# Kernel optimization log

Measured on AMD Instinct MI355X. Metric: run time of the kernel, lower is better.

## Reference

```python
import jax, jax.numpy as jnp
import numpy as np


def lga_once(x, w, r):
    """One pass of local guided aggregation (GANet LGA).

    x: [B, D, H, W] cost volume
    w: [B, 3*k*k, H, W] per-pixel guidance weights (k = 2r+1); the three
       k*k groups weight disparity planes d, d-1, d+1 respectively.
    out[b,d,h,w] = sum_{i,j in kxk window}
        w0[b,ij,h,w] * x[b, d,   h+i-r, w+j-r]
      + w1[b,ij,h,w] * x[b, d-1, h+i-r, w+j-r]
      + w2[b,ij,h,w] * x[b, d+1, h+i-r, w+j-r]
    with zero padding outside spatial and disparity bounds.
    """
    B, D, H, W = x.shape
    k = 2 * r + 1
    k2 = k * k
    w0 = w[:, 0 * k2:1 * k2]
    w1 = w[:, 1 * k2:2 * k2]
    w2 = w[:, 2 * k2:3 * k2]
    # disparity-shifted volumes: xm[:, d] = x[:, d-1], xp[:, d] = x[:, d+1]
    xm = jnp.pad(x, ((0, 0), (1, 0), (0, 0), (0, 0)))[:, :D]
    xp = jnp.pad(x, ((0, 0), (0, 1), (0, 0), (0, 0)))[:, 1:]
    spad = ((0, 0), (0, 0), (r, r), (r, r))
    x0p = jnp.pad(x, spad)
    xmp = jnp.pad(xm, spad)
    xpp = jnp.pad(xp, spad)
    out = jnp.zeros_like(x)
    idx = 0
    for i in range(k):          # small fixed kxk loop; data dims stay vectorized
        for j in range(k):
            p0 = x0p[:, :, i:i + H, j:j + W]
            pm = xmp[:, :, i:i + H, j:j + W]
            pp = xpp[:, :, i:i + H, j:j + W]
            out = out + (w0[:, idx:idx + 1] * p0
                         + w1[:, idx:idx + 1] * pm
                         + w2[:, idx:idx + 1] * pp)
            idx += 1
    return out


def setup_inputs() -> dict:
    key = jax.random.key(0)
    k1, k2 = jax.random.split(key)
    B, D, H, W = 2, 48, 320, 640
    r = 2
    kk = 2 * r + 1
    input1 = jax.random.normal(k1, (B, D, H, W), dtype=jnp.float32)
    input2 = jax.random.uniform(k2, (B, 3 * kk * kk, H, W), dtype=jnp.float32)
    return {"input1": input1, "input2": input2, "radius": r}


def reference(input1, input2, radius):
    # LGA2 = local guided aggregation applied twice with the same weights
    y = lga_once(input1, input2, radius)
    return lga_once(y, input2, radius)
```

## Files before the change

### kernel.cpp

```cpp
#include <hip/hip_runtime.h>

namespace {
constexpr int Bn = 2, Dn = 48, Hn = 320, Wn = 640;
constexpr int R = 2, K = 5, K2 = 25, C3 = 75;
constexpr int TW = 64, TH = 4;
constexpr int LW = TW + 2 * R;
constexpr int LH = TH + 2 * R;
constexpr int NT = TW * TH;
constexpr int LTOT = LH * LW;
constexpr int NCH = 3;
constexpr int NSLOT = 4;
}

__global__ __launch_bounds__(NT, 2)
void lga_pass(const float* __restrict__ x, const float* __restrict__ wt,
              float* __restrict__ out) {
    __shared__ float pl[NSLOT][LTOT];

    const int tx = threadIdx.x;
    const int ty = threadIdx.y;
    const int tid = ty * TW + tx;

    const int w0pix = blockIdx.x * TW;
    const int h0pix = blockIdx.y * TH;
    const int b = blockIdx.z;

    const int gw = w0pix + tx;
    const int gh = h0pix + ty;

    const size_t ps = (size_t)Hn * Wn;

    int  soff[NCH];
    bool sval[NCH];
#pragma unroll
    for (int t = 0; t < NCH; ++t) {
        int idx = tid + t * NT;
        int rr = idx / LW;
        int cc = idx - rr * LW;
        int hh = h0pix - R + rr;
        int ww = w0pix - R + cc;
        bool ok = (idx < LTOT) && hh >= 0 && hh < Hn && ww >= 0 && ww < Wn;
        sval[t] = ok;
        soff[t] = ok ? (hh * Wn + ww) : 0;
    }

    const float* xb = x + (size_t)b * Dn * ps;

    float wr[C3];
    {
        const float* wp = wt + (size_t)b * C3 * ps + (size_t)gh * Wn + gw;
#pragma unroll
        for (int c = 0; c < C3; ++c) wr[c] = wp[(size_t)c * ps];
    }

    float* op = out + (size_t)b * Dn * ps + (size_t)gh * Wn + gw;
    const int lbase = ty * LW + tx;

    auto issue = [&](int p, float (&g)[NCH]) {
        const float* src = xb + (size_t)p * ps;
        const bool pv = p < Dn;
#pragma unroll
        for (int t = 0; t < NCH; ++t)
            g[t] = (pv && sval[t]) ? src[soff[t]] : 0.f;
    };
    auto commit = [&](int slot, const float (&g)[NCH]) {
#pragma unroll
        for (int t = 0; t < NCH; ++t) {
            int idx = tid + t * NT;
            if (t < NCH - 1 || idx < LTOT) pl[slot][idx] = g[t];
        }
    };

    float carry = 0.f, s1prev = 0.f;

    auto step = [&](int p, int sR, int sC,
                    float (&gI)[NCH], const float (&gC)[NCH]) {
        issue(p + 4, gI);
        float S0 = 0.f, S1 = 0.f, S2 = 0.f;
#pragma unroll
        for (int i = 0; i < K; ++i) {
            float v0 = pl[sR][lbase + i * LW + 0];
            float v1 = pl[sR][lbase + i * LW + 1];
            float v2 = pl[sR][lbase + i * LW + 2];
            float v3 = pl[sR][lbase + i * LW + 3];
            float v4 = pl[sR][lbase + i * LW + 4];
            S0 += wr[i*K+0]*v0 + wr[i*K+1]*v1 + wr[i*K+2]*v2 + wr[i*K+3]*v3 + wr[i*K+4]*v4;
            S1 += wr[K2+i*K+0]*v0 + wr[K2+i*K+1]*v1 + wr[K2+i*K+2]*v2 + wr[K2+i*K+3]*v3 + wr[K2+i*K+4]*v4;
            S2 += wr[2*K2+i*K+0]*v0 + wr[2*K2+i*K+1]*v1 + wr[2*K2+i*K+2]*v2 + wr[2*K2+i*K+3]*v3 + wr[2*K2+i*K+4]*v4;
        }
        commit(sC, gC);
        if (p > 0) { *op = carry + S2; op += ps; }
        carry = S0 + s1prev;
        s1prev = S1;
    };

    float G0[NCH], G1[NCH], G2[NCH];
    {
        float t[NCH];
        issue(0, t); commit(0, t);
        issue(1, t); commit(1, t);
    }
    issue(2, G1);
    issue(3, G2);
    __syncthreads();

    for (int d0 = 0; d0 < Dn; d0 += 12) {
        step(d0 + 0, 0, 2, G0, G1);
        step(d0 + 1, 1, 3, G1, G2);
        __syncthreads();
        step(d0 + 2, 2, 0, G2, G0);
        step(d0 + 3, 3, 1, G0, G1);
        __syncthreads();
        step(d0 + 4, 0, 2, G1, G2);
        step(d0 + 5, 1, 3, G2, G0);
        __syncthreads();
        step(d0 + 6, 2, 0, G0, G1);
        step(d0 + 7, 3, 1, G1, G2);
        __syncthreads();
        step(d0 + 8, 0, 2, G2, G0);
        step(d0 + 9, 1, 3, G0, G1);
        __syncthreads();
        step(d0 + 10, 2, 0, G1, G2);
        step(d0 + 11, 3, 1, G2, G0);
        if (d0 + 12 < Dn) __syncthreads();
    }
    *op = carry;
}

extern "C" void kernel_launch(void* const* d_in, const int* in_sizes, int n_in,
                              void* d_out, int out_size, void* d_ws, size_t ws_size,
                              hipStream_t stream) {
    const float* x = (const float*)d_in[0];
    const float* w = (const float*)d_in[1];
    float* out = (float*)d_out;
    float* tmp = (float*)d_ws;

    dim3 block(TW, TH, 1);
    dim3 grid(Wn / TW, Hn / TH, Bn);

    lga_pass<<<grid, block, 0, stream>>>(x, w, tmp);
    lga_pass<<<grid, block, 0, stream>>>(tmp, w, out);
}
```

Measured before the change: 467.1 us.

## Stream halo tiles directly into LDS with async global_load_lds pipeline

Replaces register-staged global loads plus LDS stores with direct global-to-LDS async loads (global_load_lds) into an 8-slot ring buffer, prefetching six planes ahead. Barriers are hand-written with s_waitcnt vmcnt counts so outstanding loads can stay in flight across steps. Out-of-bounds handling moves from masking the loaded values to zeroing the corresponding weights, so halo slots can hold arbitrary data. This removes VGPR staging and ds_write instructions and deepens latency hiding, at the cost of doubled LDS use and fragile manual vmcnt accounting.

After: 380.4 us. -18.5%, faster.

```diff
diff --git a/kernel.cpp b/kernel.cpp
--- a/kernel.cpp
+++ b/kernel.cpp
@@ -8,14 +8,17 @@
 constexpr int LH = TH + 2 * R;
 constexpr int NT = TW * TH;
 constexpr int LTOT = LH * LW;
-constexpr int NCH = 3;
-constexpr int NSLOT = 4;
+constexpr int LTOTP = 576;
+constexpr int NSLOT = 8;
 }
+
+#define BARRIER(N) \
+    asm volatile("s_waitcnt vmcnt(" #N ") lgkmcnt(0)\n\ts_barrier" ::: "memory")
 
 __global__ __launch_bounds__(NT, 2)
 void lga_pass(const float* __restrict__ x, const float* __restrict__ wt,
               float* __restrict__ out) {
-    __shared__ float pl[NSLOT][LTOT];
+    __shared__ __align__(16) float pl[NSLOT][LTOTP];
 
     const int tx = threadIdx.x;
     const int ty = threadIdx.y;
@@ -30,52 +33,68 @@
 
     const size_t ps = (size_t)Hn * Wn;
 
-    int  soff[NCH];
-    bool sval[NCH];
+    int soff[3];
 #pragma unroll
-    for (int t = 0; t < NCH; ++t) {
+    for (int t = 0; t < 3; ++t) {
         int idx = tid + t * NT;
         int rr = idx / LW;
         int cc = idx - rr * LW;
         int hh = h0pix - R + rr;
         int ww = w0pix - R + cc;
         bool ok = (idx < LTOT) && hh >= 0 && hh < Hn && ww >= 0 && ww < Wn;
-        sval[t] = ok;
         soff[t] = ok ? (hh * Wn + ww) : 0;
     }
 
     const float* xb = x + (size_t)b * Dn * ps;
+    const int wseg = tid & ~63;
 
     float wr[C3];
     {
         const float* wp = wt + (size_t)b * C3 * ps + (size_t)gh * Wn + gw;
 #pragma unroll
         for (int c = 0; c < C3; ++c) wr[c] = wp[(size_t)c * ps];
+#pragma unroll
+        for (int i = 0; i < K; ++i) {
+            const int hh = gh + i - R;
+            const bool vh = (hh >= 0) && (hh < Hn);
+#pragma unroll
+            for (int j = 0; j < K; ++j) {
+                const int ww = gw + j - R;
+                if (!(vh && ww >= 0 && ww < Wn)) {
+                    wr[i * K + j] = 0.f;
+                    wr[K2 + i * K + j] = 0.f;
+                    wr[2 * K2 + i * K + j] = 0.f;
+                }
+            }
+        }
     }
 
     float* op = out + (size_t)b * Dn * ps + (size_t)gh * Wn + gw;
     const int lbase = ty * LW + tx;
 
-    auto issue = [&](int p, float (&g)[NCH]) {
+    auto dma = [&](int p, int slot) {
+        if (p >= Dn) return;
         const float* src = xb + (size_t)p * ps;
-        const bool pv = p < Dn;
-#pragma unroll
-        for (int t = 0; t < NCH; ++t)
-            g[t] = (pv && sval[t]) ? src[soff[t]] : 0.f;
-    };
-    auto commit = [&](int slot, const float (&g)[NCH]) {
-#pragma unroll
-        for (int t = 0; t < NCH; ++t) {
-            int idx = tid + t * NT;
-            if (t < NCH - 1 || idx < LTOT) pl[slot][idx] = g[t];
+        __builtin_amdgcn_global_load_lds(
+            (const __attribute__((address_space(1))) void*)(src + soff[0]),
+            (__attribute__((address_space(3))) void*)(&pl[slot][0 * NT + wseg]),
+            4, 0, 0);
+        __builtin_amdgcn_global_load_lds(
+            (const __attribute__((address_space(1))) void*)(src + soff[1]),
+            (__attribute__((address_space(3))) void*)(&pl[slot][1 * NT + wseg]),
+            4, 0, 0);
+        if (ty == 0) {
+            __builtin_amdgcn_global_load_lds(
+                (const __attribute__((address_space(1))) void*)(src + soff[2]),
+                (__attribute__((address_space(3))) void*)(&pl[slot][2 * NT + tx]),
+                4, 0, 0);
         }
     };
 
     float carry = 0.f, s1prev = 0.f;
 
-    auto step = [&](int p, int sR, int sC,
-                    float (&gI)[NCH], const float (&gC)[NCH]) {
-        issue(p + 4, gI);
+    auto step = [&](int p, int sR, int sD) {
+        dma(p + 6, sD);
         float S0 = 0.f, S1 = 0.f, S2 = 0.f;
 #pragma unroll
         for (int i = 0; i < K; ++i) {
@@ -88,42 +107,25 @@
             S1 += wr[K2+i*K+0]*v0 + wr[K2+i*K+1]*v1 + wr[K2+i*K+2]*v2 + wr[K2+i*K+3]*v3 + wr[K2+i*K+4]*v4;
             S2 += wr[2*K2+i*K+0]*v0 + wr[2*K2+i*K+1]*v1 + wr[2*K2+i*K+2]*v2 + wr[2*K2+i*K+3]*v3 + wr[2*K2+i*K+4]*v4;
         }
-        commit(sC, gC);
         if (p > 0) { *op = carry + S2; op += ps; }
         carry = S0 + s1prev;
         s1prev = S1;
     };
 
-    float G0[NCH], G1[NCH], G2[NCH];
-    {
-        float t[NCH];
-        issue(0, t); commit(0, t);
-        issue(1, t); commit(1, t);
+#pragma unroll
+    for (int q = 0; q < 6; ++q) dma(q, q);
+    BARRIER(8);
+
+    for (int d0 = 0; d0 < 40; d0 += 8) {
+        step(d0 + 0, 0, 6); step(d0 + 1, 1, 7); BARRIER(8);
+        step(d0 + 2, 2, 0); step(d0 + 3, 3, 1); BARRIER(8);
+        step(d0 + 4, 4, 2); step(d0 + 5, 5, 3); BARRIER(8);
+        step(d0 + 6, 6, 4); step(d0 + 7, 7, 5); BARRIER(8);
     }
-    issue(2, G1);
-    issue(3, G2);
-    __syncthreads();
-
-    for (int d0 = 0; d0 < Dn; d0 += 12) {
-        step(d0 + 0, 0, 2, G0, G1);
-        step(d0 + 1, 1, 3, G1, G2);
-        __syncthreads();
-        step(d0 + 2, 2, 0, G2, G0);
-        step(d0 + 3, 3, 1, G0, G1);
-        __syncthreads();
-        step(d0 + 4, 0, 2, G1, G2);
-        step(d0 + 5, 1, 3, G2, G0);
-        __syncthreads();
-        step(d0 + 6, 2, 0, G0, G1);
-        step(d0 + 7, 3, 1, G1, G2);
-        __syncthreads();
-        step(d0 + 8, 0, 2, G2, G0);
-        step(d0 + 9, 1, 3, G0, G1);
-        __syncthreads();
-        step(d0 + 10, 2, 0, G1, G2);
-        step(d0 + 11, 3, 1, G2, G0);
-        if (d0 + 12 < Dn) __syncthreads();
-    }
+    step(40, 0, 6); step(41, 1, 7); BARRIER(8);
+    step(42, 2, 0); step(43, 3, 1); BARRIER(4);
+    step(44, 4, 2); step(45, 5, 3); BARRIER(0);
+    step(46, 6, 4); step(47, 7, 5);
     *op = carry;
 }
 
```
